# Performance work log

Measured on AMD Instinct MI355X. Metric: run time of the kernel, lower is better.

The kernel has to match this reference:

```python
import jax, jax.numpy as jnp
import numpy as np

B, S1, S2 = 8, 2048, 2048
K1_DIM = K2_DIM = 512
PK1_DIM = PK2_DIM = 256
ATT_DIM = 512
DV = 512


def setup_inputs() -> dict:
    key = jax.random.key(0)
    ks = jax.random.split(key, 16)
    s = 0.02
    inp = {
        "k1": jax.random.normal(ks[0], (B, S1, K1_DIM), jnp.float32),
        "k2": jax.random.normal(ks[1], (B, S2, K2_DIM), jnp.float32),
        "preserved_k1": jax.random.normal(ks[2], (B, S1, PK1_DIM), jnp.float32),
        "preserved_k2": jax.random.normal(ks[3], (B, S2, PK2_DIM), jnp.float32),
        "v1": jax.random.normal(ks[4], (B, S1, DV), jnp.float32),
        "v2": jax.random.normal(ks[5], (B, S2, DV), jnp.float32),
        # Linear params stored as [in, out] (x @ W + b == torch Linear)
        "W_k1": jax.random.normal(ks[6], (K1_DIM, ATT_DIM), jnp.float32) * s,
        "b_k1": jnp.zeros((ATT_DIM,), jnp.float32),
        "W_k2": jax.random.normal(ks[7], (K2_DIM, ATT_DIM), jnp.float32) * s,
        "b_k2": jnp.zeros((ATT_DIM,), jnp.float32),
        "W_pk1": jax.random.normal(ks[8], (K1_DIM + PK1_DIM, ATT_DIM), jnp.float32) * s,
        "b_pk1": jnp.zeros((ATT_DIM,), jnp.float32),
        "W_pk2": jax.random.normal(ks[9], (K2_DIM + PK2_DIM, ATT_DIM), jnp.float32) * s,
        "b_pk2": jnp.zeros((ATT_DIM,), jnp.float32),
        # lengths in [S/2, S) so no softmax row is fully masked (original exits on NaN)
        "k1_lengths": jax.random.randint(ks[10], (B,), S1 // 2, S1, jnp.int32).astype(jnp.int64),
        "k2_lengths": jax.random.randint(ks[11], (B,), S2 // 2, S2, jnp.int32).astype(jnp.int64),
    }
    return inp


def _mask(k1_lengths, k2_lengths):
    # Faithful to the original loop: a position is masked iff EXACTLY ONE of
    # (row >= l1) / (col >= l2) holds (mask counter == 1, not >= 1).
    row_over = (jnp.arange(S1)[None, :, None] >= k1_lengths[:, None, None])  # [B,S1,1]
    col_over = (jnp.arange(S2)[None, None, :] >= k2_lengths[:, None, None])  # [B,1,S2]
    return (row_over.astype(jnp.int32) + col_over.astype(jnp.int32)) == 1  # [B,S1,S2]


def reference(k1, k2, preserved_k1, preserved_k2, v1, v2,
              W_k1, b_k1, W_k2, b_k2, W_pk1, b_pk1, W_pk2, b_pk2,
              k1_lengths, k2_lengths):
    pk1 = jnp.concatenate([k1, preserved_k1], axis=-1) @ W_pk1 + b_pk1  # [B,S1,A]
    pk2 = jnp.concatenate([k2, preserved_k2], axis=-1) @ W_pk2 + b_pk2  # [B,S2,A]
    k1p = k1 @ W_k1 + b_k1  # [B,S1,A]
    k2p = k2 @ W_k2 + b_k2  # [B,S2,A]

    score_1 = jnp.einsum("bsa,bta->bst", k1p, pk2)   # [B,S1,S2]
    score_2 = jnp.einsum("bsa,bta->bst", pk1, k2p)   # [B,S1,S2]

    mask = _mask(k1_lengths, k2_lengths)
    score_1 = jnp.where(mask, -jnp.inf, score_1)
    score_2 = jnp.where(mask, -jnp.inf, score_2)

    w1 = jax.nn.softmax(jnp.swapaxes(score_1, 1, 2), axis=-1)  # [B,S2,S1]
    w2 = jax.nn.softmax(score_2, axis=-1)                      # [B,S1,S2]

    o1 = jnp.einsum("bts,bsd->btd", w1, v1)  # [B,S2,DV]
    o2 = jnp.einsum("bst,btd->bsd", w2, v2)  # [B,S1,DV]
    # NOTE: original returns ragged per-sample slices of w1/w2; we return the
    # full padded weight matrices (slice w1[i,:l2,:l1], w2[i,:l1,:l2] to match).
    return (o1, o2, w1, w2)
```

## Files before the change

### kernel.cpp

```cpp
#include <hip/hip_runtime.h>

typedef _Float16 half8 __attribute__((ext_vector_type(8)));
typedef float    floatx4 __attribute__((ext_vector_type(4)));
typedef unsigned short u16;

constexpr int Bn  = 8;
constexpr int Sq  = 2048;
constexpr int KD  = 512;
constexpr int PKD = 256;
constexpr int AD  = 512;
constexpr int DV  = 512;

__device__ __forceinline__ void llds16(const void* g, void* l)
{
    __builtin_amdgcn_global_load_lds(
        (const __attribute__((address_space(1))) unsigned int*)g,
        (__attribute__((address_space(3))) unsigned int*)l, 16, 0, 0);
}

__global__ __launch_bounds__(256)
void transpose_cast_k(const float* __restrict__ in0, const float* __restrict__ in1,
                      _Float16* __restrict__ out0, _Float16* __restrict__ out1,
                      int inRows, int inCols, long long bsIn, long long bsOut,
                      int zsplit)
{
    __shared__ float t[32][33];
    const int bz = blockIdx.z;
    const bool sel = (bz >= zsplit);
    const int b = sel ? bz - zsplit : bz;
    const float* in = (sel ? in1 : in0) + (long long)b * bsIn;
    _Float16* out = (sel ? out1 : out0) + (long long)b * bsOut;
    const int tx = threadIdx.x & 31;
    const int ty = threadIdx.x >> 5;
    const int c0 = blockIdx.x * 32;
    const int r0 = blockIdx.y * 32;
#pragma unroll
    for (int i = 0; i < 4; ++i)
        t[ty + 8*i][tx] = in[(long long)(r0 + ty + 8*i) * inCols + c0 + tx];
    __syncthreads();
#pragma unroll
    for (int i = 0; i < 4; ++i)
        out[(long long)(c0 + ty + 8*i) * inRows + r0 + tx] = (_Float16)t[tx][ty + 8*i];
}

__global__ __launch_bounds__(256)
void wT_all_k(const float* __restrict__ Wk1, const float* __restrict__ Wk2,
              const float* __restrict__ Wpk1, const float* __restrict__ Wpk2,
              _Float16* __restrict__ Tk1, _Float16* __restrict__ Tk2,
              _Float16* __restrict__ Tpk1, _Float16* __restrict__ Tpk2)
{
    const int z = blockIdx.z;
    const float* W; _Float16* T; int Krows;
    if      (z == 0) { W = Wk1;  T = Tk1;  Krows = KD; }
    else if (z == 1) { W = Wk2;  T = Tk2;  Krows = KD; }
    else if (z == 2) { W = Wpk1; T = Tpk1; Krows = KD + PKD; }
    else             { W = Wpk2; T = Tpk2; Krows = KD + PKD; }
    const int r0 = blockIdx.y * 32;
    if (r0 >= Krows) return;
    const int c0 = blockIdx.x * 32;
    __shared__ float t[32][33];
    const int tx = threadIdx.x & 31;
    const int ty = threadIdx.x >> 5;
#pragma unroll
    for (int i = 0; i < 4; ++i)
        t[ty + 8*i][tx] = W[(long long)(r0 + ty + 8*i) * AD + c0 + tx];
    __syncthreads();
#pragma unroll
    for (int i = 0; i < 4; ++i)
        T[(long long)(c0 + ty + 8*i) * Krows + r0 + tx] = (_Float16)t[tx][ty + 8*i];
}

__global__ __launch_bounds__(256)
void cast_cat_k(const float* __restrict__ x0, const float* __restrict__ y0,
                _Float16* __restrict__ o0,
                const float* __restrict__ x1, const float* __restrict__ y1,
                _Float16* __restrict__ o1)
{
    const bool sel = (blockIdx.z != 0);
    const float* x = sel ? x1 : x0;
    const float* y = sel ? y1 : y0;
    _Float16* out = sel ? o1 : o0;
    const int idx = blockIdx.x * 256 + threadIdx.x;
    const int e   = idx * 8;
    const int r   = e / 768;
    const int c   = e % 768;
    const float* src = (c < 512) ? (x + (long long)r * 512 + c)
                                 : (y + (long long)r * 256 + (c - 512));
    const floatx4 f0 = *(const floatx4*)(src);
    const floatx4 f1 = *(const floatx4*)(src + 4);
    half8 h;
#pragma unroll
    for (int j = 0; j < 4; ++j) { h[j] = (_Float16)f0[j]; h[4 + j] = (_Float16)f1[j]; }
    *(half8*)(out + (long long)e) = h;
}

template<bool A_F32, bool OUT_F16>
__global__ __launch_bounds__(256, 2)
void gemm_k(const void* __restrict__ A1v, const void* __restrict__ A2v, int Ksplit,
            int lda1, int lda2, long long bsA,
            const _Float16* __restrict__ Bm, int ldb, long long bsB,
            void* __restrict__ Cv, int ldc, long long bsC,
            const float* __restrict__ bias, int K)
{
    __shared__ __align__(16) unsigned char AsRaw[A_F32 ? 16384 : 8192];
    __shared__ __align__(16) unsigned char BsRaw[8192];

    const int tid  = threadIdx.x;
    const int lane = tid & 63;
    const int wave = tid >> 6;
    const int wm   = (wave >> 1) * 64;
    const int wn   = (wave & 1) * 64;
    const int fr   = lane & 15;
    const int fq   = lane >> 4;

    const int tm = blockIdx.y, tn = blockIdx.x, bz = blockIdx.z;
    const long long aRowBase = (long long)tm * 128;
    const long long bRowBase = (long long)tn * 128;
    const _Float16* Bbase = Bm + (long long)bz * bsB;

    floatx4 acc[4][4];
#pragma unroll
    for (int i = 0; i < 4; ++i)
#pragma unroll
        for (int j = 0; j < 4; ++j) acc[i][j] = (floatx4)0.0f;

    for (int k0 = 0; k0 < K; k0 += 32) {
        __syncthreads();

        if (A_F32) {
            const float* A1 = (const float*)A1v + (long long)bz * bsA;
            const float* A2 = (const float*)A2v;
#pragma unroll
            for (int is = 0; is < 4; ++is) {
                const int r  = (tid >> 3) + is * 32;
                const int ch = (tid & 7) ^ (r & 7);
                const int kk = k0 + ch * 4;
                const float* src = (kk < Ksplit)
                    ? A1 + (aRowBase + r) * lda1 + kk
                    : A2 + (aRowBase + r) * lda2 + (kk - Ksplit);
                llds16(src, AsRaw + tid * 16 + is * 4096);
            }
        } else {
            const _Float16* A1 = (const _Float16*)A1v + (long long)bz * bsA;
#pragma unroll
            for (int is = 0; is < 2; ++is) {
                const int r  = (tid >> 2) + is * 64;
                const int ch = (tid & 3) ^ (r & 3);
                llds16(A1 + (aRowBase + r) * lda1 + k0 + ch * 8,
                       AsRaw + tid * 16 + is * 4096);
            }
        }
#pragma unroll
        for (int is = 0; is < 2; ++is) {
            const int r  = (tid >> 2) + is * 64;
            const int ch = (tid & 3) ^ (r & 3);
            llds16(Bbase + (bRowBase + r) * ldb + k0 + ch * 8,
                   BsRaw + tid * 16 + is * 4096);
        }

        __syncthreads();

        half8 af[4], bf[4];
        if (A_F32) {
            const float* As32 = (const float*)AsRaw;
#pragma unroll
            for (int i = 0; i < 4; ++i) {
                const int r  = wm + i * 16 + fr;
                const int c0 = ((2 * fq) ^ (r & 7)) * 4;
                const int c1 = ((2 * fq + 1) ^ (r & 7)) * 4;
                floatx4 f0 = *(const floatx4*)(As32 + r * 32 + c0);
                floatx4 f1 = *(const floatx4*)(As32 + r * 32 + c1);
                half8 h;
#pragma unroll
                for (int j = 0; j < 4; ++j) {
                    h[j]     = (_Float16)f0[j];
                    h[4 + j] = (_Float16)f1[j];
                }
                af[i] = h;
            }
        } else {
            const _Float16* As16 = (const _Float16*)AsRaw;
#pragma unroll
            for (int i = 0; i < 4; ++i) {
                const int r  = wm + i * 16 + fr;
                const int ch = fq ^ (r & 3);
                af[i] = *(const half8*)(As16 + r * 32 + ch * 8);
            }
        }
        {
            const _Float16* Bs16 = (const _Float16*)BsRaw;
#pragma unroll
            for (int j = 0; j < 4; ++j) {
                const int r  = wn + j * 16 + fr;
                const int ch = fq ^ (r & 3);
                bf[j] = *(const half8*)(Bs16 + r * 32 + ch * 8);
            }
        }
#pragma unroll
        for (int i = 0; i < 4; ++i)
#pragma unroll
            for (int j = 0; j < 4; ++j)
                acc[i][j] = __builtin_amdgcn_mfma_f32_16x16x32_f16(af[i], bf[j], acc[i][j], 0, 0, 0);
    }

    const int crow0 = tm * 128 + wm + fq * 4;
    const int ccol0 = tn * 128 + wn + fr;
    if (OUT_F16) {
        _Float16* C = (_Float16*)Cv + (long long)bz * bsC;
#pragma unroll
        for (int i = 0; i < 4; ++i)
#pragma unroll
            for (int j = 0; j < 4; ++j) {
                const int col = ccol0 + j * 16;
                const float bv = bias[col];
#pragma unroll
                for (int r = 0; r < 4; ++r)
                    C[(long long)(crow0 + i*16 + r) * ldc + col] = (_Float16)(acc[i][j][r] + bv);
            }
    } else {
        float* C = (float*)Cv + (long long)bz * bsC;
#pragma unroll
        for (int i = 0; i < 4; ++i)
#pragma unroll
            for (int j = 0; j < 4; ++j) {
                const int col = ccol0 + j * 16;
#pragma unroll
                for (int r = 0; r < 4; ++r)
                    C[(long long)(crow0 + i*16 + r) * ldc + col] = acc[i][j][r];
            }
    }
}

template<bool OUT16>
__global__ __launch_bounds__(512, 2)
void gemm256_k(const _Float16* __restrict__ A0, const _Float16* __restrict__ A1,
               const _Float16* __restrict__ B0, const _Float16* __restrict__ B1,
               void* __restrict__ C0v, void* __restrict__ C1v,
               long long bsA, int lda, long long bsB, int ldb,
               long long bsC, int ldc, int K, int zsplit)
{
    __shared__ __align__(16) _Float16 lds[65536];

    const int nwg  = 64 * gridDim.z;
    const int lin0 = (blockIdx.z * 8 + blockIdx.y) * 8 + blockIdx.x;
    const int cpx  = nwg >> 3;
    const int lin  = (lin0 & 7) * cpx + (lin0 >> 3);
    const int tn   = lin & 7;
    const int tm   = (lin >> 3) & 7;
    const int bz   = lin >> 6;

    const bool sel = (bz >= zsplit);
    const int  bzl = sel ? (bz - zsplit) : bz;
    const _Float16* Am = sel ? A1 : A0;
    const _Float16* Bm = sel ? B1 : B0;

    const int tid  = threadIdx.x;
    const int lane = tid & 63;
    const int wave = tid >> 6;
    const int wm   = (wave >> 2) * 128;
    const int wn   = (wave & 3) * 64;
    const int fr   = lane & 15;
    const int fq   = lane >> 4;

    const _Float16* Ab = Am + (long long)bzl * bsA + (long long)tm * 256 * lda;
    const _Float16* Bb = Bm + (long long)bzl * bsB + (long long)tn * 256 * ldb;

    const int sr = lane >> 3;
    const int ch = (lane & 7) ^ sr;
    const _Float16* srcA[2][2];
    const _Float16* srcB[2][2];
#pragma unroll
    for (int h = 0; h < 2; ++h)
#pragma unroll
        for (int l = 0; l < 2; ++l) {
            const int r = h * 128 + (wave * 2 + l) * 8 + sr;
            srcA[h][l] = Ab + (long long)r * lda + ch * 8;
            srcB[h][l] = Bb + (long long)r * ldb + ch * 8;
        }

    auto stageA = [&](int kt, int buf) {
#pragma unroll
        for (int h = 0; h < 2; ++h)
#pragma unroll
            for (int l = 0; l < 2; ++l)
                llds16(srcA[h][l] + kt * 64,
                       lds + buf * 32768 + h * 8192 + (wave * 2 + l) * 512 + lane * 8);
    };
    auto stageB = [&](int kt, int buf) {
#pragma unroll
        for (int h = 0; h < 2; ++h)
#pragma unroll
            for (int l = 0; l < 2; ++l)
                llds16(srcB[h][l] + kt * 64,
                       lds + buf * 32768 + 16384 + h * 8192 + (wave * 2 + l) * 512 + lane * 8);
    };

    auto rdA = [&](int buf, int im, int kk) -> half8 {
        const int row = wm + im * 16 + fr;
        const int c   = (kk * 4 + fq) ^ (row & 7);
        return *(const half8*)(lds + buf * 32768 + row * 64 + c * 8);
    };
    auto rdB = [&](int buf, int jn, int kk) -> half8 {
        const int row = wn + jn * 16 + fr;
        const int c   = (kk * 4 + fq) ^ (row & 7);
        return *(const half8*)(lds + buf * 32768 + 16384 + row * 64 + c * 8);
    };

    floatx4 acc[8][4];
#pragma unroll
    for (int i = 0; i < 8; ++i)
#pragma unroll
        for (int j = 0; j < 4; ++j) acc[i][j] = (floatx4)0.0f;

    const int KT = K >> 6;

    stageA(0, 0);
    stageB(0, 0);
    __syncthreads();

    for (int kt = 0; kt < KT; ++kt) {
        const int buf = kt & 1;
        half8 af[4][2], bf[2][2];
#pragma unroll
        for (int q = 0; q < 4; ++q) {
            const int nh = q >> 1;
            const int mh = (q == 1 || q == 2) ? 1 : 0;
            if (q == 0 || q == 2) {
#pragma unroll
                for (int j = 0; j < 2; ++j)
#pragma unroll
                    for (int kk = 0; kk < 2; ++kk)
                        bf[j][kk] = rdB(buf, nh * 2 + j, kk);
            }
            if (q != 2) {
#pragma unroll
                for (int i = 0; i < 4; ++i)
#pragma unroll
                    for (int kk = 0; kk < 2; ++kk)
                        af[i][kk] = rdA(buf, mh * 4 + i, kk);
            }
            if (kt + 1 < KT) {
                if (q == 0)      stageA(kt + 1, buf ^ 1);
                else if (q == 1) stageB(kt + 1, buf ^ 1);
            }
            __builtin_amdgcn_s_barrier();
            __builtin_amdgcn_s_setprio(1);
#pragma unroll
            for (int i = 0; i < 4; ++i)
#pragma unroll
                for (int j = 0; j < 2; ++j)
#pragma unroll
                    for (int kk = 0; kk < 2; ++kk)
                        acc[mh * 4 + i][nh * 2 + j] =
                            __builtin_amdgcn_mfma_f32_16x16x32_f16(
                                af[i][kk], bf[j][kk], acc[mh * 4 + i][nh * 2 + j], 0, 0, 0);
            __builtin_amdgcn_s_setprio(0);
            if (q < 3) __builtin_amdgcn_s_barrier();
        }
        __syncthreads();
    }

    const int crow0 = tm * 256 + wm + fq * 4;
    const int ccol0 = tn * 256 + wn + fr;
    if (OUT16) {
        _Float16* Cb = (_Float16*)(sel ? C1v : C0v) + (long long)bzl * bsC;
#pragma unroll
        for (int i = 0; i < 8; ++i)
#pragma unroll
            for (int j = 0; j < 4; ++j) {
                const long long base = (long long)(crow0 + i * 16) * ldc + ccol0 + j * 16;
#pragma unroll
                for (int r = 0; r < 4; ++r)
                    Cb[base + (long long)r * ldc] = (_Float16)acc[i][j][r];
            }
    } else {
        float* Cb = (float*)(sel ? C1v : C0v) + (long long)bzl * bsC;
#pragma unroll
        for (int i = 0; i < 8; ++i)
#pragma unroll
            for (int j = 0; j < 4; ++j) {
                const long long base = (long long)(crow0 + i * 16) * ldc + ccol0 + j * 16;
#pragma unroll
                for (int r = 0; r < 4; ++r)
                    Cb[base + (long long)r * ldc] = acc[i][j][r];
            }
    }
}

template<bool OUT_F16>
__global__ __launch_bounds__(512, 2)
void gemm256x128_k(const _Float16* __restrict__ A0, const _Float16* __restrict__ A1,
                   long long bsA, int lda,
                   const _Float16* __restrict__ B0, const _Float16* __restrict__ B1,
                   long long bsB, int ldb,
                   void* __restrict__ C0, void* __restrict__ C1,
                   long long bsC, int ldc,
                   const float* __restrict__ bias0, const float* __restrict__ bias1,
                   int K, int zsplit)
{
    __shared__ __align__(16) _Float16 lds[73728];

    const int gx   = gridDim.x, gy = gridDim.y;
    const int nwg  = gx * gy * gridDim.z;
    const int lin0 = (blockIdx.z * gy + blockIdx.y) * gx + blockIdx.x;
    const int cpx  = nwg >> 3;
    const int lin  = (lin0 & 7) * cpx + (lin0 >> 3);
    const int tn   = lin % gx;
    const int tmp2 = lin / gx;
    const int tm   = tmp2 % gy;
    const int bz   = tmp2 / gy;

    const bool sel = (bz >= zsplit);
    const int  bzl = sel ? (bz - zsplit) : bz;
    const _Float16* Am = sel ? A1 : A0;
    const _Float16* Bm = sel ? B1 : B0;

    const int tid  = threadIdx.x;
    const int lane = tid & 63;
    const int wave = tid >> 6;
    const int wm   = (wave >> 2) * 128;
    const int wn   = (wave & 3) * 32;
    const int fr   = lane & 15;
    const int fq   = lane >> 4;

    const _Float16* Ab = Am + (long long)bzl * bsA + (long long)tm * 256 * lda;
    const _Float16* Bb = Bm + (long long)bzl * bsB + (long long)tn * 128 * ldb;

    const int sr = lane >> 3;
    const int ch = (lane & 7) ^ sr;
    const _Float16* srcA[2][2];
    const _Float16* srcB[2];
#pragma unroll
    for (int h = 0; h < 2; ++h)
#pragma unroll
        for (int l = 0; l < 2; ++l)
            srcA[h][l] = Ab + (long long)(h * 128 + (wave * 2 + l) * 8 + sr) * lda + ch * 8;
#pragma unroll
    for (int l = 0; l < 2; ++l)
        srcB[l] = Bb + (long long)((wave * 2 + l) * 8 + sr) * ldb + ch * 8;

    auto stageA = [&](int kt, int buf) {
#pragma unroll
        for (int h = 0; h < 2; ++h)
#pragma unroll
            for (int l = 0; l < 2; ++l)
                llds16(srcA[h][l] + kt * 64,
                       lds + buf * 24576 + h * 8192 + (wave * 2 + l) * 512 + lane * 8);
    };
    auto stageB = [&](int kt, int buf) {
#pragma unroll
        for (int l = 0; l < 2; ++l)
            llds16(srcB[l] + kt * 64,
                   lds + buf * 24576 + 16384 + (wave * 2 + l) * 512 + lane * 8);
    };

    auto rdA = [&](int buf, int im, int kk) -> half8 {
        const int row = wm + im * 16 + fr;
        const int c   = (kk * 4 + fq) ^ (row & 7);
        return *(const half8*)(lds + buf * 24576 + row * 64 + c * 8);
    };
    auto rdB = [&](int buf, int jn, int kk) -> half8 {
        const int row = wn + jn * 16 + fr;
        const int c   = (kk * 4 + fq) ^ (row & 7);
        return *(const half8*)(lds + buf * 24576 + 16384 + row * 64 + c * 8);
    };

    floatx4 acc[8][2];
#pragma unroll
    for (int i = 0; i < 8; ++i)
#pragma unroll
        for (int j = 0; j < 2; ++j) acc[i][j] = (floatx4)0.0f;

    const int KT = K >> 6;

    stageA(0, 0); stageB(0, 0);
    if (KT > 1) {
        stageA(1, 1); stageB(1, 1);
        asm volatile("s_waitcnt vmcnt(6)" ::: "memory");
    } else {
        asm volatile("s_waitcnt vmcnt(0)" ::: "memory");
    }
    __builtin_amdgcn_sched_barrier(0);
    __builtin_amdgcn_s_barrier();
    __builtin_amdgcn_sched_barrier(0);

    int bufR = 0, bufP = 2;
    for (int kt = 0; kt < KT; ++kt) {
        half8 afA[4][2], afB[4][2], bf0[2], bf1[2];
        const bool pf = (kt + 2 < KT);

#pragma unroll
        for (int kk = 0; kk < 2; ++kk) bf0[kk] = rdB(bufR, 0, kk);
#pragma unroll
        for (int i = 0; i < 4; ++i)
#pragma unroll
            for (int kk = 0; kk < 2; ++kk) afA[i][kk] = rdA(bufR, i, kk);
        if (pf) stageA(kt + 2, bufP);
        __builtin_amdgcn_s_barrier();
        __builtin_amdgcn_s_setprio(1);
#pragma unroll
        for (int i = 0; i < 4; ++i)
#pragma unroll
            for (int kk = 0; kk < 2; ++kk)
                acc[i][0] = __builtin_amdgcn_mfma_f32_16x16x32_f16(afA[i][kk], bf0[kk], acc[i][0], 0, 0, 0);
        __builtin_amdgcn_s_setprio(0);
        __builtin_amdgcn_s_barrier();

#pragma unroll
        for (int i = 0; i < 4; ++i)
#pragma unroll
            for (int kk = 0; kk < 2; ++kk) afB[i][kk] = rdA(bufR, 4 + i, kk);
        if (pf) stageB(kt + 2, bufP);
        __builtin_amdgcn_s_barrier();
        __builtin_amdgcn_s_setprio(1);
#pragma unroll
        for (int i = 0; i < 4; ++i)
#pragma unroll
            for (int kk = 0; kk < 2; ++kk)
                acc[4 + i][0] = __builtin_amdgcn_mfma_f32_16x16x32_f16(afB[i][kk], bf0[kk], acc[4 + i][0], 0, 0, 0);
        __builtin_amdgcn_s_setprio(0);
        __builtin_amdgcn_s_barrier();

#pragma unroll
        for (int kk = 0; kk < 2; ++kk) bf1[kk] = rdB(bufR, 1, kk);
        __builtin_amdgcn_s_barrier();
        __builtin_amdgcn_s_setprio(1);
#pragma unroll
        for (int i = 0; i < 4; ++i)
#pragma unroll
            for (int kk = 0; kk < 2; ++kk)
                acc[4 + i][1] = __builtin_amdgcn_mfma_f32_16x16x32_f16(afB[i][kk], bf1[kk], acc[4 + i][1], 0, 0, 0);
        __builtin_amdgcn_s_setprio(0);
        __builtin_amdgcn_s_barrier();

        __builtin_amdgcn_s_setprio(1);
#pragma unroll
        for (int i = 0; i < 4; ++i)
#pragma unroll
            for (int kk = 0; kk < 2; ++kk)
                acc[i][1] = __builtin_amdgcn_mfma_f32_16x16x32_f16(afA[i][kk], bf1[kk], acc[i][1], 0, 0, 0);
        __builtin_amdgcn_s_setprio(0);

        if (kt + 1 < KT) {
            if (pf) asm volatile("s_waitcnt vmcnt(6)" ::: "memory");
            else    asm volatile("s_waitcnt vmcnt(0)" ::: "memory");
            __builtin_amdgcn_sched_barrier(0);
            __builtin_amdgcn_s_barrier();
            __builtin_amdgcn_sched_barrier(0);
        }
        bufR = (bufR == 2) ? 0 : bufR + 1;
        bufP = (bufP == 2) ? 0 : bufP + 1;
    }

    const int crow0 = tm * 256 + wm + fq * 4;
    const int ccol0 = tn * 128 + wn + fr;
    if (OUT_F16) {
        const float* bias = sel ? bias1 : bias0;
        _Float16* C = (_Float16*)(sel ? C1 : C0) + (long long)bzl * bsC;
#pragma unroll
        for (int i = 0; i < 8; ++i)
#pragma unroll
            for (int j = 0; j < 2; ++j) {
                const int col = ccol0 + j * 16;
                const float bv = bias[col];
#pragma unroll
                for (int r = 0; r < 4; ++r)
                    C[(long long)(crow0 + i * 16 + r) * ldc + col] = (_Float16)(acc[i][j][r] + bv);
            }
    } else {
        float* C = (float*)(sel ? C1 : C0) + (long long)bzl * bsC;
#pragma unroll
        for (int i = 0; i < 8; ++i)
#pragma unroll
            for (int j = 0; j < 2; ++j) {
                const int col = ccol0 + j * 16;
#pragma unroll
                for (int r = 0; r < 4; ++r)
                    C[(long long)(crow0 + i * 16 + r) * ldc + col] = acc[i][j][r];
            }
    }
}

__global__ __launch_bounds__(512, 2)
void gemm_proj_k(const _Float16* __restrict__ Acat1, const _Float16* __restrict__ Acat2,
                 const _Float16* __restrict__ B0, const _Float16* __restrict__ B1,
                 const _Float16* __restrict__ B2, const _Float16* __restrict__ B3,
                 _Float16* __restrict__ C0, _Float16* __restrict__ C1,
                 _Float16* __restrict__ C2, _Float16* __restrict__ C3,
                 const float* __restrict__ bias0, const float* __restrict__ bias1,
                 const float* __restrict__ bias2, const float* __restrict__ bias3,
                 int K0, int K1)
{
    __shared__ __align__(16) _Float16 lds[73728];

    const int nwg  = 4 * 64 * 4;
    const int lin0 = (blockIdx.z * 64 + blockIdx.y) * 4 + blockIdx.x;
    const int cpx  = nwg >> 3;
    const int lin  = (lin0 & 7) * cpx + (lin0 >> 3);
    const int tn   = lin & 3;
    const int tm   = (lin >> 2) & 63;
    const int pz   = lin >> 8;

    const _Float16* Am = (pz & 1) ? Acat2 : Acat1;
    const _Float16* Bm; _Float16* Cm; const float* bias; int K;
    if      (pz == 0) { Bm = B0; Cm = C0; bias = bias0; K = K0; }
    else if (pz == 1) { Bm = B1; Cm = C1; bias = bias1; K = K0; }
    else if (pz == 2) { Bm = B2; Cm = C2; bias = bias2; K = K1; }
    else              { Bm = B3; Cm = C3; bias = bias3; K = K1; }
    const int lda = KD + PKD;
    const int ldb = K;
    const int ldc = AD;

    const int tid  = threadIdx.x;
    const int lane = tid & 63;
    const int wave = tid >> 6;
    const int wm   = (wave >> 2) * 128;
    const int wn   = (wave & 3) * 32;
    const int fr   = lane & 15;
    const int fq   = lane >> 4;

    const _Float16* Ab = Am + (long long)tm * 256 * lda;
    const _Float16* Bb = Bm + (long long)tn * 128 * ldb;

    const int sr = lane >> 3;
    const int ch = (lane & 7) ^ sr;
    const _Float16* srcA[2][2];
    const _Float16* srcB[2];
#pragma unroll
    for (int h = 0; h < 2; ++h)
#pragma unroll
        for (int l = 0; l < 2; ++l)
            srcA[h][l] = Ab + (long long)(h * 128 + (wave * 2 + l) * 8 + sr) * lda + ch * 8;
#pragma unroll
    for (int l = 0; l < 2; ++l)
        srcB[l] = Bb + (long long)((wave * 2 + l) * 8 + sr) * ldb + ch * 8;

    auto stageA = [&](int kt, int buf) {
#pragma unroll
        for (int h = 0; h < 2; ++h)
#pragma unroll
            for (int l = 0; l < 2; ++l)
                llds16(srcA[h][l] + kt * 64,
                       lds + buf * 24576 + h * 8192 + (wave * 2 + l) * 512 + lane * 8);
    };
    auto stageB = [&](int kt, int buf) {
#pragma unroll
        for (int l = 0; l < 2; ++l)
            llds16(srcB[l] + kt * 64,
                   lds + buf * 24576 + 16384 + (wave * 2 + l) * 512 + lane * 8);
    };

    auto rdA = [&](int buf, int im, int kk) -> half8 {
        const int row = wm + im * 16 + fr;
        const int c   = (kk * 4 + fq) ^ (row & 7);
        return *(const half8*)(lds + buf * 24576 + row * 64 + c * 8);
    };
    auto rdB = [&](int buf, int jn, int kk) -> half8 {
        const int row = wn + jn * 16 + fr;
        const int c   = (kk * 4 + fq) ^ (row & 7);
        return *(const half8*)(lds + buf * 24576 + 16384 + row * 64 + c * 8);
    };

    floatx4 acc[8][2];
#pragma unroll
    for (int i = 0; i < 8; ++i)
#pragma unroll
        for (int j = 0; j < 2; ++j) acc[i][j] = (floatx4)0.0f;

    const int KT = K >> 6;

    stageA(0, 0); stageB(0, 0);
    if (KT > 1) {
        stageA(1, 1); stageB(1, 1);
        asm volatile("s_waitcnt vmcnt(6)" ::: "memory");
    } else {
        asm volatile("s_waitcnt vmcnt(0)" ::: "memory");
    }
    __builtin_amdgcn_sched_barrier(0);
    __builtin_amdgcn_s_barrier();
    __builtin_amdgcn_sched_barrier(0);

    int bufR = 0, bufP = 2;
    for (int kt = 0; kt < KT; ++kt) {
        half8 afA[4][2], afB[4][2], bf0[2], bf1[2];
        const bool pf = (kt + 2 < KT);

#pragma unroll
        for (int kk = 0; kk < 2; ++kk) bf0[kk] = rdB(bufR, 0, kk);
#pragma unroll
        for (int i = 0; i < 4; ++i)
#pragma unroll
            for (int kk = 0; kk < 2; ++kk) afA[i][kk] = rdA(bufR, i, kk);
        if (pf) stageA(kt + 2, bufP);
        __builtin_amdgcn_s_barrier();
        __builtin_amdgcn_s_setprio(1);
#pragma unroll
        for (int i = 0; i < 4; ++i)
#pragma unroll
            for (int kk = 0; kk < 2; ++kk)
                acc[i][0] = __builtin_amdgcn_mfma_f32_16x16x32_f16(afA[i][kk], bf0[kk], acc[i][0], 0, 0, 0);
        __builtin_amdgcn_s_setprio(0);
        __builtin_amdgcn_s_barrier();

#pragma unroll
        for (int i = 0; i < 4; ++i)
#pragma unroll
            for (int kk = 0; kk < 2; ++kk) afB[i][kk] = rdA(bufR, 4 + i, kk);
        if (pf) stageB(kt + 2, bufP);
        __builtin_amdgcn_s_barrier();
        __builtin_amdgcn_s_setprio(1);
#pragma unroll
        for (int i = 0; i < 4; ++i)
#pragma unroll
            for (int kk = 0; kk < 2; ++kk)
                acc[4 + i][0] = __builtin_amdgcn_mfma_f32_16x16x32_f16(afB[i][kk], bf0[kk], acc[4 + i][0], 0, 0, 0);
        __builtin_amdgcn_s_setprio(0);
        __builtin_amdgcn_s_barrier();

#pragma unroll
        for (int kk = 0; kk < 2; ++kk) bf1[kk] = rdB(bufR, 1, kk);
        __builtin_amdgcn_s_barrier();
        __builtin_amdgcn_s_setprio(1);
#pragma unroll
        for (int i = 0; i < 4; ++i)
#pragma unroll
            for (int kk = 0; kk < 2; ++kk)
                acc[4 + i][1] = __builtin_amdgcn_mfma_f32_16x16x32_f16(afB[i][kk], bf1[kk], acc[4 + i][1], 0, 0, 0);
        __builtin_amdgcn_s_setprio(0);
        __builtin_amdgcn_s_barrier();

        __builtin_amdgcn_s_setprio(1);
#pragma unroll
        for (int i = 0; i < 4; ++i)
#pragma unroll
            for (int kk = 0; kk < 2; ++kk)
                acc[i][1] = __builtin_amdgcn_mfma_f32_16x16x32_f16(afA[i][kk], bf1[kk], acc[i][1], 0, 0, 0);
        __builtin_amdgcn_s_setprio(0);

        if (kt + 1 < KT) {
            if (pf) asm volatile("s_waitcnt vmcnt(6)" ::: "memory");
            else    asm volatile("s_waitcnt vmcnt(0)" ::: "memory");
            __builtin_amdgcn_sched_barrier(0);
            __builtin_amdgcn_s_barrier();
            __builtin_amdgcn_sched_barrier(0);
        }
        bufR = (bufR == 2) ? 0 : bufR + 1;
        bufP = (bufP == 2) ? 0 : bufP + 1;
    }

    const int crow0 = tm * 256 + wm + fq * 4;
    const int ccol0 = tn * 128 + wn + fr;
#pragma unroll
    for (int i = 0; i < 8; ++i)
#pragma unroll
        for (int j = 0; j < 2; ++j) {
            const int col = ccol0 + j * 16;
            const float bv = bias[col];
#pragma unroll
            for (int r = 0; r < 4; ++r)
                Cm[(long long)(crow0 + i * 16 + r) * ldc + col] = (_Float16)(acc[i][j][r] + bv);
        }
}

__device__ __forceinline__ int load_len(const int* __restrict__ p, int b)
{
    return (p[1] == 0) ? p[2 * b] : p[b];
}

template<bool F16IN>
__global__ __launch_bounds__(256)
void softmax_mask_k(float* __restrict__ w1p, float* __restrict__ w2p,
                    _Float16* __restrict__ wh1, _Float16* __restrict__ wh2,
                    const int* __restrict__ len1, const int* __restrict__ len2)
{
    const int z = blockIdx.z;
    float* w = z ? w2p : w1p;
    _Float16* wh = z ? wh2 : wh1;
    const int* lenR = z ? len1 : len2;
    const int* lenC = z ? len2 : len1;

    const int b = blockIdx.y;
    const int r = blockIdx.x;
    const long long rowOff = ((long long)b * Sq + r) * (long long)Sq;
    float* row = w + rowOff;
    const int lr = load_len(lenR, b);
    const int lc = load_len(lenC, b);
    const bool rover = (r >= lr);
    const int tid  = threadIdx.x;
    const int lane = tid & 63;
    const int wave = tid >> 6;

    float v[8];
    if (F16IN) {
        const half8 hv = *(const half8*)(wh + rowOff + tid * 8);
#pragma unroll
        for (int j = 0; j < 8; ++j) v[j] = (float)hv[j];
    } else {
        const floatx4 x0 = *(const floatx4*)(row + tid * 8);
        const floatx4 x1 = *(const floatx4*)(row + tid * 8 + 4);
#pragma unroll
        for (int j = 0; j < 4; ++j) { v[j] = x0[j]; v[4 + j] = x1[j]; }
    }

    float m = -3.0e38f;
#pragma unroll
    for (int j = 0; j < 8; ++j) {
        const int c = tid * 8 + j;
        if (rover != (c >= lc)) v[j] = -__builtin_inff();
        m = fmaxf(m, v[j]);
    }
#pragma unroll
    for (int off = 32; off > 0; off >>= 1) m = fmaxf(m, __shfl_xor(m, off, 64));
    __shared__ float redm[4], reds[4];
    if (lane == 0) redm[wave] = m;
    __syncthreads();
    m = fmaxf(fmaxf(redm[0], redm[1]), fmaxf(redm[2], redm[3]));

    float s = 0.f;
#pragma unroll
    for (int j = 0; j < 8; ++j) { v[j] = __expf(v[j] - m); s += v[j]; }
#pragma unroll
    for (int off = 32; off > 0; off >>= 1) s += __shfl_xor(s, off, 64);
    if (lane == 0) reds[wave] = s;
    __syncthreads();
    s = reds[0] + reds[1] + reds[2] + reds[3];
    const float inv = 1.0f / s;

    floatx4 x0, x1;
#pragma unroll
    for (int j = 0; j < 4; ++j) { x0[j] = v[j] * inv; x1[j] = v[4 + j] * inv; }
    *(floatx4*)(row + tid * 8)     = x0;
    *(floatx4*)(row + tid * 8 + 4) = x1;
    if (F16IN || wh != nullptr) {
        half8 h;
#pragma unroll
        for (int j = 0; j < 4; ++j) { h[j] = (_Float16)x0[j]; h[4 + j] = (_Float16)x1[j]; }
        *(half8*)(wh + rowOff + tid * 8) = h;
    }
}

extern "C" void kernel_launch(void* const* d_in, const int* in_sizes, int n_in,
                              void* d_out, int out_size, void* d_ws, size_t ws_size,
                              hipStream_t stream)
{
    (void)in_sizes; (void)n_in; (void)out_size;
    const float* k1    = (const float*)d_in[0];
    const float* k2    = (const float*)d_in[1];
    const float* pk1in = (const float*)d_in[2];
    const float* pk2in = (const float*)d_in[3];
    const float* v1    = (const float*)d_in[4];
    const float* v2    = (const float*)d_in[5];
    const float* W_k1  = (const float*)d_in[6];
    const float* b_k1  = (const float*)d_in[7];
    const float* W_k2  = (const float*)d_in[8];
    const float* b_k2  = (const float*)d_in[9];
    const float* W_pk1 = (const float*)d_in[10];
    const float* b_pk1 = (const float*)d_in[11];
    const float* W_pk2 = (const float*)d_in[12];
    const float* b_pk2 = (const float*)d_in[13];
    const int* len1 = (const int*)d_in[14];
    const int* len2 = (const int*)d_in[15];

    float* out = (float*)d_out;
    float* o1 = out;
    float* o2 = o1 + (long long)Bn * Sq * DV;
    float* w1 = o2 + (long long)Bn * Sq * DV;
    float* w2 = w1 + (long long)Bn * Sq * Sq;

    _Float16* k1p = (_Float16*)o1;
    _Float16* k2p = k1p + (long long)Bn * Sq * AD;
    _Float16* pk1 = (_Float16*)o2;
    _Float16* pk2 = pk1 + (long long)Bn * Sq * AD;
    _Float16* cat1 = pk2 + (long long)Bn * Sq * AD;
    _Float16* cat2 = cat1 + (long long)Bn * Sq * (KD + PKD);

    _Float16* vT1   = (_Float16*)d_ws;
    _Float16* vT2   = vT1 + (long long)Bn * DV * Sq;
    _Float16* WTk1  = vT2 + (long long)Bn * DV * Sq;
    _Float16* WTk2  = WTk1 + AD * KD;
    _Float16* WTpk1 = WTk2 + AD * KD;
    _Float16* WTpk2 = WTpk1 + AD * (KD + PKD);

    const unsigned long long fixedHalves =
        2ull * Bn * DV * Sq + 2ull * AD * KD + 2ull * AD * (KD + PKD);
    _Float16* w1h = (_Float16*)d_ws + fixedHalves;
    _Float16* w2h = w1h + (long long)Bn * Sq * Sq;
    const bool fast =
        ws_size >= (fixedHalves + 2ull * Bn * Sq * Sq) * sizeof(_Float16);

    wT_all_k<<<dim3(AD/32, (KD+PKD)/32, 4), 256, 0, stream>>>(
        W_k1, W_k2, W_pk1, W_pk2, WTk1, WTk2, WTpk1, WTpk2);
    transpose_cast_k<<<dim3(DV/32, Sq/32, 2*Bn), 256, 0, stream>>>(
        v1, v2, vT1, vT2, Sq, DV, (long long)Sq*DV, (long long)Sq*DV, Bn);
    cast_cat_k<<<dim3((Bn*Sq*(KD+PKD))/(256*8), 1, 2), 256, 0, stream>>>(
        k1, pk1in, cat1, k2, pk2in, cat2);

    gemm_proj_k<<<dim3(AD/128, (Bn*Sq)/256, 4), 512, 0, stream>>>(
        cat1, cat2,
        WTk1, WTk2, WTpk1, WTpk2,
        k1p, k2p, pk1, pk2,
        b_k1, b_k2, b_pk1, b_pk2,
        KD, KD + PKD);

    if (fast) {
        gemm256_k<true><<<dim3(Sq/256, Sq/256, 2*Bn), 512, 0, stream>>>(
            pk2, pk1, k1p, k2p, w1h, w2h,
            (long long)Sq*AD, AD, (long long)Sq*AD, AD,
            (long long)Sq*Sq, Sq, AD, Bn);
    } else {
        gemm256_k<false><<<dim3(Sq/256, Sq/256, 2*Bn), 512, 0, stream>>>(
            pk2, pk1, k1p, k2p, w1, w2,
            (long long)Sq*AD, AD, (long long)Sq*AD, AD,
            (long long)Sq*Sq, Sq, AD, Bn);
    }

    if (fast) {
        softmax_mask_k<true><<<dim3(Sq, Bn, 2), 256, 0, stream>>>(
            w1, w2, w1h, w2h, len1, len2);
    } else {
        softmax_mask_k<false><<<dim3(Sq, Bn, 2), 256, 0, stream>>>(
            w1, w2, nullptr, nullptr, len1, len2);
    }

    if (fast) {
        gemm256x128_k<false><<<dim3(DV/128, Sq/256, 2*Bn), 512, 0, stream>>>(
            w1h, w2h, (long long)Sq*Sq, Sq,
            vT1, vT2, (long long)DV*Sq, Sq,
            o1, o2, (long long)Sq*DV, DV,
            nullptr, nullptr, Sq, Bn);
    } else {
        const dim3 gOut(DV/128, Sq/128, Bn);
        gemm_k<true, false><<<gOut, 256, 0, stream>>>(
            w1, w1, Sq, Sq, Sq, (long long)Sq*Sq,
            vT1, Sq, (long long)DV*Sq,
            o1, DV, (long long)Sq*DV, nullptr, Sq);
        gemm_k<true, false><<<gOut, 256, 0, stream>>>(
            w2, w2, Sq, Sq, Sq, (long long)Sq*Sq,
            vT2, Sq, (long long)DV*Sq,
            o2, DV, (long long)Sq*DV, nullptr, Sq);
    }
}
```

Baseline: 767.8 us.

## Use 256x256 tiles for output GEMM and nontemporal stores for score and softmax writes

```diff
diff --git a/kernel.cpp b/kernel.cpp
--- a/kernel.cpp
+++ b/kernel.cpp
@@ -241,13 +241,15 @@
 {
     __shared__ __align__(16) _Float16 lds[65536];
 
-    const int nwg  = 64 * gridDim.z;
-    const int lin0 = (blockIdx.z * 8 + blockIdx.y) * 8 + blockIdx.x;
+    const int gx   = gridDim.x, gy = gridDim.y;
+    const int nwg  = gx * gy * gridDim.z;
+    const int lin0 = (blockIdx.z * gy + blockIdx.y) * gx + blockIdx.x;
     const int cpx  = nwg >> 3;
     const int lin  = (lin0 & 7) * cpx + (lin0 >> 3);
-    const int tn   = lin & 7;
-    const int tm   = (lin >> 3) & 7;
-    const int bz   = lin >> 6;
+    const int tn   = lin % gx;
+    const int tmp2 = lin / gx;
+    const int tm   = tmp2 % gy;
+    const int bz   = tmp2 / gy;
 
     const bool sel = (bz >= zsplit);
     const int  bzl = sel ? (bz - zsplit) : bz;
@@ -382,38 +384,41 @@
                 const long long base = (long long)(crow0 + i * 16) * ldc + ccol0 + j * 16;
 #pragma unroll
                 for (int r = 0; r < 4; ++r)
-                    Cb[base + (long long)r * ldc] = acc[i][j][r];
-            }
-    }
-}
-
-template<bool OUT_F16>
+                    __builtin_nontemporal_store(acc[i][j][r],
+                        &Cb[base + (long long)r * ldc]);
+            }
+    }
+}
+
 __global__ __launch_bounds__(512, 2)
-void gemm256x128_k(const _Float16* __restrict__ A0, const _Float16* __restrict__ A1,
-                   long long bsA, int lda,
-                   const _Float16* __restrict__ B0, const _Float16* __restrict__ B1,
-                   long long bsB, int ldb,
-                   void* __restrict__ C0, void* __restrict__ C1,
-                   long long bsC, int ldc,
-                   const float* __restrict__ bias0, const float* __restrict__ bias1,
-                   int K, int zsplit)
+void gemm_proj_k(const _Float16* __restrict__ Acat1, const _Float16* __restrict__ Acat2,
+                 const _Float16* __restrict__ B0, const _Float16* __restrict__ B1,
+                 const _Float16* __restrict__ B2, const _Float16* __restrict__ B3,
+                 _Float16* __restrict__ C0, _Float16* __restrict__ C1,
+                 _Float16* __restrict__ C2, _Float16* __restrict__ C3,
+                 const float* __restrict__ bias0, const float* __restrict__ bias1,
+                 const float* __restrict__ bias2, const float* __restrict__ bias3,
+                 int K0, int K1)
 {
     __shared__ __align__(16) _Float16 lds[73728];
 
-    const int gx   = gridDim.x, gy = gridDim.y;
-    const int nwg  = gx * gy * gridDim.z;
-    const int lin0 = (blockIdx.z * gy + blockIdx.y) * gx + blockIdx.x;
+    const int nwg  = 4 * 64 * 4;
+    const int lin0 = (blockIdx.z * 64 + blockIdx.y) * 4 + blockIdx.x;
     const int cpx  = nwg >> 3;
     const int lin  = (lin0 & 7) * cpx + (lin0 >> 3);
-    const int tn   = lin % gx;
-    const int tmp2 = lin / gx;
-    const int tm   = tmp2 % gy;
-    const int bz   = tmp2 / gy;
-
-    const bool sel = (bz >= zsplit);
-    const int  bzl = sel ? (bz - zsplit) : bz;
-    const _Float16* Am = sel ? A1 : A0;
-    const _Float16* Bm = sel ? B1 : B0;
+    const int tn   = lin & 3;
+    const int tm   = (lin >> 2) & 63;
+    const int pz   = lin >> 8;
+
+    const _Float16* Am = (pz & 1) ? Acat2 : Acat1;
+    const _Float16* Bm; _Float16* Cm; const float* bias; int K;
+    if      (pz == 0) { Bm = B0; Cm = C0; bias = bias0; K = K0; }
+    else if (pz == 1) { Bm = B1; Cm = C1; bias = bias1; K = K0; }
+    else if (pz == 2) { Bm = B2; Cm = C2; bias = bias2; K = K1; }
+    else              { Bm = B3; Cm = C3; bias = bias3; K = K1; }
+    const int lda = KD + PKD;
+    const int ldb = K;
+    const int ldc = AD;
 
     const int tid  = threadIdx.x;
     const int lane = tid & 63;
@@ -423,8 +428,8 @@
     const int fr   = lane & 15;
     const int fq   = lane >> 4;
 
-    const _Float16* Ab = Am + (long long)bzl * bsA + (long long)tm * 256 * lda;
-    const _Float16* Bb = Bm + (long long)bzl * bsB + (long long)tn * 128 * ldb;
+    const _Float16* Ab = Am + (long long)tm * 256 * lda;
+    const _Float16* Bb = Bm + (long long)tn * 128 * ldb;
 
     const int sr = lane >> 3;
     const int ch = (lane & 7) ^ sr;
@@ -554,202 +559,6 @@
 
     const int crow0 = tm * 256 + wm + fq * 4;
     const int ccol0 = tn * 128 + wn + fr;
-    if (OUT_F16) {
-        const float* bias = sel ? bias1 : bias0;
-        _Float16* C = (_Float16*)(sel ? C1 : C0) + (long long)bzl * bsC;
-#pragma unroll
-        for (int i = 0; i < 8; ++i)
-#pragma unroll
-            for (int j = 0; j < 2; ++j) {
-                const int col = ccol0 + j * 16;
-                const float bv = bias[col];
-#pragma unroll
-                for (int r = 0; r < 4; ++r)
-                    C[(long long)(crow0 + i * 16 + r) * ldc + col] = (_Float16)(acc[i][j][r] + bv);
-            }
-    } else {
-        float* C = (float*)(sel ? C1 : C0) + (long long)bzl * bsC;
-#pragma unroll
-        for (int i = 0; i < 8; ++i)
-#pragma unroll
-            for (int j = 0; j < 2; ++j) {
-                const int col = ccol0 + j * 16;
-#pragma unroll
-                for (int r = 0; r < 4; ++r)
-                    C[(long long)(crow0 + i * 16 + r) * ldc + col] = acc[i][j][r];
-            }
-    }
-}
-
-__global__ __launch_bounds__(512, 2)
-void gemm_proj_k(const _Float16* __restrict__ Acat1, const _Float16* __restrict__ Acat2,
-                 const _Float16* __restrict__ B0, const _Float16* __restrict__ B1,
-                 const _Float16* __restrict__ B2, const _Float16* __restrict__ B3,
-                 _Float16* __restrict__ C0, _Float16* __restrict__ C1,
-                 _Float16* __restrict__ C2, _Float16* __restrict__ C3,
-                 const float* __restrict__ bias0, const float* __restrict__ bias1,
-                 const float* __restrict__ bias2, const float* __restrict__ bias3,
-                 int K0, int K1)
-{
-    __shared__ __align__(16) _Float16 lds[73728];
-
-    const int nwg  = 4 * 64 * 4;
-    const int lin0 = (blockIdx.z * 64 + blockIdx.y) * 4 + blockIdx.x;
-    const int cpx  = nwg >> 3;
-    const int lin  = (lin0 & 7) * cpx + (lin0 >> 3);
-    const int tn   = lin & 3;
-    const int tm   = (lin >> 2) & 63;
-    const int pz   = lin >> 8;
-
-    const _Float16* Am = (pz & 1) ? Acat2 : Acat1;
-    const _Float16* Bm; _Float16* Cm; const float* bias; int K;
-    if      (pz == 0) { Bm = B0; Cm = C0; bias = bias0; K = K0; }
-    else if (pz == 1) { Bm = B1; Cm = C1; bias = bias1; K = K0; }
-    else if (pz == 2) { Bm = B2; Cm = C2; bias = bias2; K = K1; }
-    else              { Bm = B3; Cm = C3; bias = bias3; K = K1; }
-    const int lda = KD + PKD;
-    const int ldb = K;
-    const int ldc = AD;
-
-    const int tid  = threadIdx.x;
-    const int lane = tid & 63;
-    const int wave = tid >> 6;
-    const int wm   = (wave >> 2) * 128;
-    const int wn   = (wave & 3) * 32;
-    const int fr   = lane & 15;
-    const int fq   = lane >> 4;
-
-    const _Float16* Ab = Am + (long long)tm * 256 * lda;
-    const _Float16* Bb = Bm + (long long)tn * 128 * ldb;
-
-    const int sr = lane >> 3;
-    const int ch = (lane & 7) ^ sr;
-    const _Float16* srcA[2][2];
-    const _Float16* srcB[2];
-#pragma unroll
-    for (int h = 0; h < 2; ++h)
-#pragma unroll
-        for (int l = 0; l < 2; ++l)
-            srcA[h][l] = Ab + (long long)(h * 128 + (wave * 2 + l) * 8 + sr) * lda + ch * 8;
-#pragma unroll
-    for (int l = 0; l < 2; ++l)
-        srcB[l] = Bb + (long long)((wave * 2 + l) * 8 + sr) * ldb + ch * 8;
-
-    auto stageA = [&](int kt, int buf) {
-#pragma unroll
-        for (int h = 0; h < 2; ++h)
-#pragma unroll
-            for (int l = 0; l < 2; ++l)
-                llds16(srcA[h][l] + kt * 64,
-                       lds + buf * 24576 + h * 8192 + (wave * 2 + l) * 512 + lane * 8);
-    };
-    auto stageB = [&](int kt, int buf) {
-#pragma unroll
-        for (int l = 0; l < 2; ++l)
-            llds16(srcB[l] + kt * 64,
-                   lds + buf * 24576 + 16384 + (wave * 2 + l) * 512 + lane * 8);
-    };
-
-    auto rdA = [&](int buf, int im, int kk) -> half8 {
-        const int row = wm + im * 16 + fr;
-        const int c   = (kk * 4 + fq) ^ (row & 7);
-        return *(const half8*)(lds + buf * 24576 + row * 64 + c * 8);
-    };
-    auto rdB = [&](int buf, int jn, int kk) -> half8 {
-        const int row = wn + jn * 16 + fr;
-        const int c   = (kk * 4 + fq) ^ (row & 7);
-        return *(const half8*)(lds + buf * 24576 + 16384 + row * 64 + c * 8);
-    };
-
-    floatx4 acc[8][2];
-#pragma unroll
-    for (int i = 0; i < 8; ++i)
-#pragma unroll
-        for (int j = 0; j < 2; ++j) acc[i][j] = (floatx4)0.0f;
-
-    const int KT = K >> 6;
-
-    stageA(0, 0); stageB(0, 0);
-    if (KT > 1) {
-        stageA(1, 1); stageB(1, 1);
-        asm volatile("s_waitcnt vmcnt(6)" ::: "memory");
-    } else {
-        asm volatile("s_waitcnt vmcnt(0)" ::: "memory");
-    }
-    __builtin_amdgcn_sched_barrier(0);
-    __builtin_amdgcn_s_barrier();
-    __builtin_amdgcn_sched_barrier(0);
-
-    int bufR = 0, bufP = 2;
-    for (int kt = 0; kt < KT; ++kt) {
-        half8 afA[4][2], afB[4][2], bf0[2], bf1[2];
-        const bool pf = (kt + 2 < KT);
-
-#pragma unroll
-        for (int kk = 0; kk < 2; ++kk) bf0[kk] = rdB(bufR, 0, kk);
-#pragma unroll
-        for (int i = 0; i < 4; ++i)
-#pragma unroll
-            for (int kk = 0; kk < 2; ++kk) afA[i][kk] = rdA(bufR, i, kk);
-        if (pf) stageA(kt + 2, bufP);
-        __builtin_amdgcn_s_barrier();
-        __builtin_amdgcn_s_setprio(1);
-#pragma unroll
-        for (int i = 0; i < 4; ++i)
-#pragma unroll
-            for (int kk = 0; kk < 2; ++kk)
-                acc[i][0] = __builtin_amdgcn_mfma_f32_16x16x32_f16(afA[i][kk], bf0[kk], acc[i][0], 0, 0, 0);
-        __builtin_amdgcn_s_setprio(0);
-        __builtin_amdgcn_s_barrier();
-
-#pragma unroll
-        for (int i = 0; i < 4; ++i)
-#pragma unroll
-            for (int kk = 0; kk < 2; ++kk) afB[i][kk] = rdA(bufR, 4 + i, kk);
-        if (pf) stageB(kt + 2, bufP);
-        __builtin_amdgcn_s_barrier();
-        __builtin_amdgcn_s_setprio(1);
-#pragma unroll
-        for (int i = 0; i < 4; ++i)
-#pragma unroll
-            for (int kk = 0; kk < 2; ++kk)
-                acc[4 + i][0] = __builtin_amdgcn_mfma_f32_16x16x32_f16(afB[i][kk], bf0[kk], acc[4 + i][0], 0, 0, 0);
-        __builtin_amdgcn_s_setprio(0);
-        __builtin_amdgcn_s_barrier();
-
-#pragma unroll
-        for (int kk = 0; kk < 2; ++kk) bf1[kk] = rdB(bufR, 1, kk);
-        __builtin_amdgcn_s_barrier();
-        __builtin_amdgcn_s_setprio(1);
-#pragma unroll
-        for (int i = 0; i < 4; ++i)
-#pragma unroll
-            for (int kk = 0; kk < 2; ++kk)
-                acc[4 + i][1] = __builtin_amdgcn_mfma_f32_16x16x32_f16(afB[i][kk], bf1[kk], acc[4 + i][1], 0, 0, 0);
-        __builtin_amdgcn_s_setprio(0);
-        __builtin_amdgcn_s_barrier();
-
-        __builtin_amdgcn_s_setprio(1);
-#pragma unroll
-        for (int i = 0; i < 4; ++i)
-#pragma unroll
-            for (int kk = 0; kk < 2; ++kk)
-                acc[i][1] = __builtin_amdgcn_mfma_f32_16x16x32_f16(afA[i][kk], bf1[kk], acc[i][1], 0, 0, 0);
-        __builtin_amdgcn_s_setprio(0);
-
-        if (kt + 1 < KT) {
-            if (pf) asm volatile("s_waitcnt vmcnt(6)" ::: "memory");
-            else    asm volatile("s_waitcnt vmcnt(0)" ::: "memory");
-            __builtin_amdgcn_sched_barrier(0);
-            __builtin_amdgcn_s_barrier();
-            __builtin_amdgcn_sched_barrier(0);
-        }
-        bufR = (bufR == 2) ? 0 : bufR + 1;
-        bufP = (bufP == 2) ? 0 : bufP + 1;
-    }
-
-    const int crow0 = tm * 256 + wm + fq * 4;
-    const int ccol0 = tn * 128 + wn + fr;
 #pragma unroll
     for (int i = 0; i < 8; ++i)
 #pragma unroll
@@ -829,8 +638,8 @@
     floatx4 x0, x1;
 #pragma unroll
     for (int j = 0; j < 4; ++j) { x0[j] = v[j] * inv; x1[j] = v[4 + j] * inv; }
-    *(floatx4*)(row + tid * 8)     = x0;
-    *(floatx4*)(row + tid * 8 + 4) = x1;
+    __builtin_nontemporal_store(x0, (floatx4*)(row + tid * 8));
+    __builtin_nontemporal_store(x1, (floatx4*)(row + tid * 8 + 4));
     if (F16IN || wh != nullptr) {
         half8 h;
 #pragma unroll
@@ -923,11 +732,10 @@
     }
 
     if (fast) {
-        gemm256x128_k<false><<<dim3(DV/128, Sq/256, 2*Bn), 512, 0, stream>>>(
-            w1h, w2h, (long long)Sq*Sq, Sq,
-            vT1, vT2, (long long)DV*Sq, Sq,
-            o1, o2, (long long)Sq*DV, DV,
-            nullptr, nullptr, Sq, Bn);
+        gemm256_k<false><<<dim3(DV/256, Sq/256, 2*Bn), 512, 0, stream>>>(
+            w1h, w2h, vT1, vT2, o1, o2,
+            (long long)Sq*Sq, Sq, (long long)DV*Sq, Sq,
+            (long long)Sq*DV, DV, Sq, Bn);
     } else {
         const dim3 gOut(DV/128, Sq/128, Bn);
         gemm_k<true, false><<<gOut, 256, 0, stream>>>(
```

After: 768.0 us. No clear change (+0.0%).
